# Kernel optimization log

Measured on AMD Instinct MI355X. Metric: run time of the kernel, lower is better.

The kernel has to match this reference:

```python
import jax, jax.numpy as jnp
import numpy as np

VOCAB = 32000
EMB = 512
HID = 1024
B = 64
LPRE = 256
MAXL = 16


def _gru(x, Wih, Whh, bih, bhh):
    # x: (B, T, E); torch GRU gate order r, z, n
    Bb, T, E = x.shape
    H = Whh.shape[1]
    xW = jnp.einsum('bte,ge->btg', x, Wih) + bih  # (B, T, 3H)
    def step(h, xt):
        gh = h @ Whh.T + bhh
        r = jax.nn.sigmoid(xt[:, :H] + gh[:, :H])
        z = jax.nn.sigmoid(xt[:, H:2 * H] + gh[:, H:2 * H])
        n = jnp.tanh(xt[:, 2 * H:] + r * gh[:, 2 * H:])
        h = (1.0 - z) * n + z * h
        return h, h
    h0 = jnp.zeros((Bb, H), x.dtype)
    hT, ys = jax.lax.scan(step, h0, jnp.swapaxes(xW, 0, 1))
    return jnp.swapaxes(ys, 0, 1), hT


def setup_inputs() -> dict:
    key = jax.random.key(0)
    ks = jax.random.split(key, 24)
    s = 0.02
    inp = {
        'pre_seq': jax.random.randint(ks[0], (B, LPRE), 0, VOCAB),
        'post_seq': jax.random.randint(ks[1], (B, LPRE), 0, VOCAB),
        'trg': jax.random.randint(ks[2], (B, MAXL), 0, 2),
        'emb': jax.random.normal(ks[3], (VOCAB, EMB), jnp.float32) * s,
        'Wih_pre': jax.random.normal(ks[4], (3 * HID, EMB), jnp.float32) * s,
        'Whh_pre': jax.random.normal(ks[5], (3 * HID, HID), jnp.float32) * s,
        'bih_pre': jnp.zeros((3 * HID,), jnp.float32),
        'bhh_pre': jnp.zeros((3 * HID,), jnp.float32),
        'Wih_post': jax.random.normal(ks[6], (3 * HID, EMB), jnp.float32) * s,
        'Whh_post': jax.random.normal(ks[7], (3 * HID, HID), jnp.float32) * s,
        'bih_post': jnp.zeros((3 * HID,), jnp.float32),
        'bhh_post': jnp.zeros((3 * HID,), jnp.float32),
        'fc_W': jax.random.normal(ks[8], (HID, 2 * HID), jnp.float32) * s,
        'fc_b': jnp.zeros((HID,), jnp.float32),
        'attn_W': jax.random.normal(ks[9], (HID, 2 * HID), jnp.float32) * s,
        'attn_b': jnp.zeros((HID,), jnp.float32),
        'v_W': jax.random.normal(ks[10], (1, HID), jnp.float32) * s,
        'fc1_W': jax.random.normal(ks[11], (HID, HID), jnp.float32) * s,
        'fc1_b': jnp.zeros((HID,), jnp.float32),
        'fc2_W': jax.random.normal(ks[12], (HID, 2 * HID), jnp.float32) * s,
        'fc2_b': jnp.zeros((HID,), jnp.float32),
        'fco_W': jax.random.normal(ks[13], (1, 2 * HID), jnp.float32) * s,
        'fco_b': jnp.zeros((1,), jnp.float32),
    }
    return inp


def reference(pre_seq, post_seq, trg, emb,
              Wih_pre, Whh_pre, bih_pre, bhh_pre,
              Wih_post, Whh_post, bih_post, bhh_post,
              fc_W, fc_b, attn_W, attn_b, v_W,
              fc1_W, fc1_b, fc2_W, fc2_b, fco_W, fco_b):
    bsz, len_pre = pre_seq.shape
    max_len = trg.shape[1]
    # Encoder (dropout = identity, eval mode)
    pre_e = emb[pre_seq]
    post_e = emb[post_seq]
    pre_out, pre_h = _gru(pre_e, Wih_pre, Whh_pre, bih_pre, bhh_pre)
    post_out, post_h = _gru(post_e, Wih_post, Whh_post, bih_post, bhh_post)
    enc_out = jnp.concatenate([pre_out, post_out], axis=1)  # (B, 2*Lp, H)
    hidden = jnp.tanh(jnp.concatenate([pre_h, post_h], axis=-1) @ fc_W.T + fc_b)  # (B, H)
    # Decoder: hidden is never updated in the original loop, so one step suffices;
    # the per-t result is identical and is broadcast over max_len.
    src_len = enc_out.shape[1]
    hid_rep = jnp.broadcast_to(hidden[:, None, :], (bsz, src_len, hidden.shape[-1]))
    energy = jnp.tanh(jnp.concatenate([hid_rep, enc_out], axis=-1) @ attn_W.T + attn_b)
    a = jax.nn.softmax(jnp.einsum('bsh,h->bs', energy, v_W[0]), axis=1)  # (B, S)
    weighted = jnp.einsum('bs,bsh->bh', a, enc_out)  # (B, H)
    o = jnp.tanh(hidden @ fc1_W.T + fc1_b)
    o = jnp.tanh(jnp.concatenate([o, weighted], axis=1) @ fc2_W.T + fc2_b)  # (B, H)
    o_rep = jnp.broadcast_to(o[:, None, :], (bsz, src_len, o.shape[-1]))
    feat = jax.nn.relu(jnp.concatenate([enc_out, o_rep], axis=-1))  # (B, S, 2H)
    logits = jnp.einsum('bsf,of->bso', feat, fco_W) + fco_b  # (B, S, 1)
    sig = jax.nn.sigmoid(logits)
    outputs_pre = jnp.broadcast_to(sig[:, None, :len_pre, :], (bsz, max_len, len_pre, 1))
    outputs_post = jnp.broadcast_to(sig[:, None, len_pre:, :], (bsz, max_len, len_pre, 1))
    return outputs_pre, outputs_post
```

## Files before the change

### kernel.cpp

```cpp
#include <hip/hip_runtime.h>
#include <math.h>

#define BATCH 64
#define LPRE 256
#define EMBD 512
#define HID 1024
#define G3 3072
#define SRC 512
#define CHUNK 32

typedef unsigned int uint32;
typedef unsigned long long u64;
typedef short bf16x8 __attribute__((ext_vector_type(8)));
typedef float f32x4 __attribute__((ext_vector_type(4)));
typedef uint32 u32x4 __attribute__((ext_vector_type(4)));

__device__ __forceinline__ float frcp_(float x) { return __builtin_amdgcn_rcpf(x); }
__device__ __forceinline__ float sigmoidf_(float x) {
    x = fminf(fmaxf(x, -30.f), 30.f);
    return frcp_(1.0f + __expf(-x));
}
__device__ __forceinline__ float tanhf_(float x) {
    x = fminf(fmaxf(x, -15.f), 15.f);
    float e = __expf(2.f * x);
    return (e - 1.f) * frcp_(e + 1.f);
}

__device__ __forceinline__ unsigned short f2bf(float f) {
    uint32 u = __float_as_uint(f);
    return (unsigned short)((u + 0x7fffu + ((u >> 16) & 1u)) >> 16);
}
__device__ __forceinline__ float bf2f(unsigned short s) { return __uint_as_float(((uint32)s) << 16); }
__device__ __forceinline__ uint4 pack8(float4 a, float4 b) {
    uint4 w;
    w.x = (uint32)f2bf(a.x) | ((uint32)f2bf(a.y) << 16);
    w.y = (uint32)f2bf(a.z) | ((uint32)f2bf(a.w) << 16);
    w.z = (uint32)f2bf(b.x) | ((uint32)f2bf(b.y) << 16);
    w.w = (uint32)f2bf(b.z) | ((uint32)f2bf(b.w) << 16);
    return w;
}

__global__ __launch_bounds__(256) void kcvt(const float* __restrict__ src, int ld, int off,
                                            unsigned short* __restrict__ dst, int cols, int n) {
    int i = blockIdx.x * 256 + threadIdx.x;
    if (i >= n) return;
    int r = i / cols, c = i - r * cols;
    dst[i] = f2bf(src[(size_t)r * ld + off + c]);
}

__global__ __launch_bounds__(256) void kproj(const int* __restrict__ pre_seq,
                                             const int* __restrict__ post_seq, int t0,
                                             const float* __restrict__ emb,
                                             const unsigned short* __restrict__ Wihb,
                                             const float* __restrict__ bih_pre,
                                             const float* __restrict__ bih_post,
                                             unsigned short* __restrict__ xw) {
    __shared__ uint4 Asl[4][128];
    __shared__ uint4 Bsl[4][128];
    __shared__ int tok[128];
    int gru = blockIdx.z;
    const int* seq = gru ? post_seq : pre_seq;
    const unsigned short* Wb = Wihb + (size_t)gru * G3 * EMBD;
    const float* bih = gru ? bih_post : bih_pre;
    unsigned short* xwout = xw + (size_t)gru * BATCH * CHUNK * G3;
    int tid = threadIdx.x;
    int row0 = blockIdx.x * 128, col0 = blockIdx.y * 128;
    if (tid < 128) {
        int rr = row0 + tid;
        tok[tid] = seq[(rr >> 5) * LPRE + t0 + (rr & 31)];
    }
    __syncthreads();
    int lane = tid & 63, w = tid >> 6;
    int wm = w >> 1, wn = w & 1;
    int q = lane >> 4, m = lane & 15;
    int r0s = tid & 127, g0s = tid >> 7;
    int g1s = g0s + 2;
    f32x4 acc[4][4] = {};
    for (int kk = 0; kk < EMBD; kk += 32) {
        const float* a0p = emb + (size_t)tok[r0s] * EMBD + kk + g0s * 8;
        const float* a1p = emb + (size_t)tok[r0s] * EMBD + kk + g1s * 8;
        float4 av00 = *(const float4*)a0p, av01 = *(const float4*)(a0p + 4);
        float4 av10 = *(const float4*)a1p, av11 = *(const float4*)(a1p + 4);
        uint4 bv0 = *(const uint4*)(Wb + (size_t)(col0 + r0s) * EMBD + kk + g0s * 8);
        uint4 bv1 = *(const uint4*)(Wb + (size_t)(col0 + r0s) * EMBD + kk + g1s * 8);
        __syncthreads();
        Asl[g0s][r0s ^ (g0s << 2)] = pack8(av00, av01);
        Asl[g1s][r0s ^ (g1s << 2)] = pack8(av10, av11);
        Bsl[g0s][r0s ^ (g0s << 2)] = bv0;
        Bsl[g1s][r0s ^ (g1s << 2)] = bv1;
        __syncthreads();
        bf16x8 af[4], bfv[4];
#pragma unroll
        for (int i = 0; i < 4; i++) af[i] = *(bf16x8*)&Asl[q][(wm * 64 + i * 16 + m) ^ (q << 2)];
#pragma unroll
        for (int j = 0; j < 4; j++) bfv[j] = *(bf16x8*)&Bsl[q][(wn * 64 + j * 16 + m) ^ (q << 2)];
#pragma unroll
        for (int i = 0; i < 4; i++)
#pragma unroll
            for (int j = 0; j < 4; j++)
                acc[i][j] = __builtin_amdgcn_mfma_f32_16x16x32_bf16(af[i], bfv[j], acc[i][j], 0, 0, 0);
    }
#pragma unroll
    for (int i = 0; i < 4; i++)
#pragma unroll
        for (int j = 0; j < 4; j++)
#pragma unroll
            for (int reg = 0; reg < 4; reg++) {
                int row = row0 + wm * 64 + i * 16 + q * 4 + reg;
                int col = col0 + wn * 64 + j * 16 + m;
                xwout[(size_t)row * G3 + col] = f2bf(acc[i][j][reg] + bih[col]);
            }
}

__global__ __launch_bounds__(512, 2) void kstepP(unsigned short* __restrict__ hbp,
                                                 float* __restrict__ hf,
                                                 const unsigned short* __restrict__ Whhb,
                                                 const float* __restrict__ bhh0,
                                                 const float* __restrict__ bhh1,
                                                 const unsigned short* __restrict__ xw,
                                                 unsigned short* __restrict__ enc,
                                                 uint32* __restrict__ bar,
                                                 int t0) {
    __shared__ float gl[8][32][3][17];
    __shared__ unsigned short hsh[32][16];
    int gru = blockIdx.z;
    int mh = blockIdx.y;
    int u0 = blockIdx.x * 16;
    int tid = threadIdx.x;
    int ks = tid >> 6;
    int lane = tid & 63;
    int q = lane >> 4, m = lane & 15;
    int bbase = mh * 32;
    const unsigned short* Wg = Whhb + (size_t)gru * G3 * HID;
    const float* bhh = gru ? bhh1 : bhh0;

    uint32* slots = bar + (size_t)gru * 128;
    uint32* gen = bar + 512 + (size_t)gru * 64;
    int sid = mh * 64 + blockIdx.x;
    bool leader = (sid == 0);

    bf16x8 bfrag[3][4];
#pragma unroll
    for (int g = 0; g < 3; ++g) {
        const unsigned short* pb = Wg + (size_t)(g * HID + u0 + m) * HID + ks * 128 + q * 8;
#pragma unroll
        for (int it = 0; it < 4; ++it) bfrag[g][it] = *(const bf16x8*)(pb + it * 32);
    }
#pragma unroll
    for (int g = 0; g < 3; ++g)
#pragma unroll
        for (int it = 0; it < 4; ++it) asm volatile("" : "+v"(bfrag[g][it]));

    int bl = tid >> 4, ul = tid & 15;
    int be = bbase + bl, ue = u0 + ul;
    float brr = bhh[ue], bzz = bhh[HID + ue], bnn = bhh[2 * HID + ue];
    unsigned short h16r = __hip_atomic_load(
        &hbp[(size_t)(((t0 & 1) * 2 + gru) * BATCH + be) * HID + ue],
        __ATOMIC_RELAXED, __HIP_MEMORY_SCOPE_AGENT);

    const unsigned short* xwb = xw + ((size_t)(gru * BATCH + be) * CHUNK) * G3;
    float xr = bf2f(xwb[ue]);
    float xz = bf2f(xwb[HID + ue]);
    float xn = bf2f(xwb[2 * HID + ue]);

    for (int tl = 0; tl < CHUNK; ++tl) {
        int t = t0 + tl;
        int p = t & 1;
        const unsigned short* hb = hbp + ((size_t)p * 2 + gru) * BATCH * HID;
        unsigned short* hob = hbp + ((size_t)(p ^ 1) * 2 + gru) * BATCH * HID;

        const unsigned short* pa0 = hb + (size_t)(bbase + m) * HID + ks * 128 + q * 8;
        const unsigned short* pa1 = pa0 + (size_t)16 * HID;
        u32x4 av0[4], av1[4];
#pragma unroll
        for (int it = 0; it < 4; ++it) {
            asm volatile("global_load_dwordx4 %0, %1, off sc0 sc1"
                         : "=v"(av0[it]) : "v"(pa0 + it * 32));
            asm volatile("global_load_dwordx4 %0, %1, off sc0 sc1"
                         : "=v"(av1[it]) : "v"(pa1 + it * 32));
        }
        asm volatile("s_waitcnt vmcnt(0)" ::: "memory");
        __builtin_amdgcn_sched_barrier(0);

        f32x4 acc[3][2] = {};
#pragma unroll
        for (int it = 0; it < 4; ++it)
#pragma unroll
            for (int g = 0; g < 3; ++g) {
                acc[g][0] = __builtin_amdgcn_mfma_f32_16x16x32_bf16(*(bf16x8*)&av0[it], bfrag[g][it], acc[g][0], 0, 0, 0);
                acc[g][1] = __builtin_amdgcn_mfma_f32_16x16x32_bf16(*(bf16x8*)&av1[it], bfrag[g][it], acc[g][1], 0, 0, 0);
            }
#pragma unroll
        for (int g = 0; g < 3; ++g)
#pragma unroll
            for (int reg = 0; reg < 4; ++reg) {
                gl[ks][q * 4 + reg][g][m] = acc[g][0][reg];
                gl[ks][16 + q * 4 + reg][g][m] = acc[g][1][reg];
            }
        __syncthreads();
        float ar = 0.f, az = 0.f, an = 0.f;
#pragma unroll
        for (int k2 = 0; k2 < 8; ++k2) {
            ar += gl[k2][bl][0][ul];
            az += gl[k2][bl][1][ul];
            an += gl[k2][bl][2][ul];
        }
        float r = sigmoidf_(xr + ar + brr);
        float z = sigmoidf_(xz + az + bzz);
        float n = tanhf_(xn + r * (an + bnn));
        float hnew = (1.f - z) * n + z * bf2f(h16r);
        unsigned short h16 = f2bf(hnew);
        h16r = h16;
        hsh[bl][ul] = h16;
        enc[((size_t)be * SRC + gru * LPRE + t) * HID + ue] = h16;
        if (t == LPRE - 1) hf[((size_t)gru * BATCH + be) * HID + ue] = hnew;
        __syncthreads();
        if (tid < 64) {
            int row = tid >> 1, half = tid & 1;
            u32x4 hv = *(const u32x4*)&hsh[row][half * 8];
            unsigned short* dst = hob + (size_t)(bbase + row) * HID + u0 + half * 8;
            asm volatile("global_store_dwordx4 %0, %1, off sc0 sc1"
                         :: "v"(dst), "v"(hv) : "memory");
        }
        if (tl < CHUNK - 1) {
            uint32 t1 = (uint32)(t + 1);
            if (tid < 64)
                asm volatile("s_waitcnt vmcnt(0)" ::: "memory");
            if (tid == 0)
                __hip_atomic_store(&slots[sid], t1, __ATOMIC_RELAXED, __HIP_MEMORY_SCOPE_AGENT);
            const unsigned short* xwn = xwb + (size_t)(tl + 1) * G3;
            xr = bf2f(xwn[ue]);
            xz = bf2f(xwn[HID + ue]);
            xn = bf2f(xwn[2 * HID + ue]);
            if (leader && tid < 64) {
                for (;;) {
                    uint32 s0 = __hip_atomic_load(&slots[tid], __ATOMIC_RELAXED, __HIP_MEMORY_SCOPE_AGENT);
                    uint32 s1 = __hip_atomic_load(&slots[tid + 64], __ATOMIC_RELAXED, __HIP_MEMORY_SCOPE_AGENT);
                    bool ok = (s0 >= t1) && (s1 >= t1);
                    if (__all(ok)) break;
                    __builtin_amdgcn_s_sleep(2);
                }
                if (tid == 0)
                    __hip_atomic_store(gen, t1, __ATOMIC_RELAXED, __HIP_MEMORY_SCOPE_AGENT);
            }
            if (tid == 0) {
                while (__hip_atomic_load(gen, __ATOMIC_RELAXED, __HIP_MEMORY_SCOPE_AGENT) < t1)
                    __builtin_amdgcn_s_sleep(2);
            }
            __syncthreads();
        }
    }
}

__global__ __launch_bounds__(256) void kg64(const float* __restrict__ A1, int K1,
                                            const float* __restrict__ A2, int K2,
                                            const unsigned short* __restrict__ Wb,
                                            const float* __restrict__ bias,
                                            float* __restrict__ out, int N, int act) {
    __shared__ uint4 Asl[4][64];
    int tid = threadIdx.x;
    int col0 = blockIdx.x * 64;
    int lane = tid & 63, w = tid >> 6;
    int q = lane >> 4, m = lane & 15;
    int K = K1 + K2;
    int arow = tid >> 2, akg = tid & 3;
    const unsigned short* wp = Wb + (size_t)(col0 + w * 16 + m) * K + q * 8;
    f32x4 acc[4] = {};
    for (int kk = 0; kk < K; kk += 32) {
        int k0 = kk + akg * 8;
        const float* ap = (k0 < K1) ? (A1 + (size_t)arow * K1 + k0)
                                    : (A2 + (size_t)arow * K2 + (k0 - K1));
        float4 v0 = *(const float4*)ap;
        float4 v1 = *(const float4*)(ap + 4);
        __syncthreads();
        Asl[akg][arow ^ (akg << 2)] = pack8(v0, v1);
        __syncthreads();
        bf16x8 bfv = *(const bf16x8*)(wp + kk);
        bf16x8 af[4];
#pragma unroll
        for (int i = 0; i < 4; i++) af[i] = *(bf16x8*)&Asl[q][(i * 16 + m) ^ (q << 2)];
#pragma unroll
        for (int i = 0; i < 4; i++)
            acc[i] = __builtin_amdgcn_mfma_f32_16x16x32_bf16(af[i], bfv, acc[i], 0, 0, 0);
    }
    int j = col0 + w * 16 + m;
    float bv = bias ? bias[j] : 0.f;
#pragma unroll
    for (int i = 0; i < 4; i++)
#pragma unroll
        for (int reg = 0; reg < 4; reg++) {
            int b = i * 16 + q * 4 + reg;
            float v = acc[i][reg] + bv;
            if (act == 1) v = tanhf_(v);
            out[(size_t)b * N + j] = v;
        }
}

__global__ __launch_bounds__(256) void kattn(const unsigned short* __restrict__ enc,
                                             const unsigned short* __restrict__ Wb,
                                             const float* __restrict__ attn_b,
                                             const float* __restrict__ hidA,
                                             const float* __restrict__ vW,
                                             float* __restrict__ e) {
    __shared__ uint4 Asl[4][128];
    __shared__ uint4 Bsl[4][128];
    __shared__ float red[2][128][17];
    int tid = threadIdx.x;
    int row0 = blockIdx.x * 128, col0 = blockIdx.y * 128;
    int lane = tid & 63, w = tid >> 6;
    int wm = w >> 1, wn = w & 1;
    int q = lane >> 4, m = lane & 15;
    int r0s = tid & 127, g0s = tid >> 7;
    int g1s = g0s + 2;
    f32x4 acc[4][4] = {};
    for (int kk = 0; kk < HID; kk += 32) {
        uint4 av0 = *(const uint4*)(enc + (size_t)(row0 + r0s) * HID + kk + g0s * 8);
        uint4 av1 = *(const uint4*)(enc + (size_t)(row0 + r0s) * HID + kk + g1s * 8);
        uint4 bv0 = *(const uint4*)(Wb + (size_t)(col0 + r0s) * HID + kk + g0s * 8);
        uint4 bv1 = *(const uint4*)(Wb + (size_t)(col0 + r0s) * HID + kk + g1s * 8);
        __syncthreads();
        Asl[g0s][r0s ^ (g0s << 2)] = av0;
        Asl[g1s][r0s ^ (g1s << 2)] = av1;
        Bsl[g0s][r0s ^ (g0s << 2)] = bv0;
        Bsl[g1s][r0s ^ (g1s << 2)] = bv1;
        __syncthreads();
        bf16x8 af[4], bfv[4];
#pragma unroll
        for (int i = 0; i < 4; i++) af[i] = *(bf16x8*)&Asl[q][(wm * 64 + i * 16 + m) ^ (q << 2)];
#pragma unroll
        for (int j = 0; j < 4; j++) bfv[j] = *(bf16x8*)&Bsl[q][(wn * 64 + j * 16 + m) ^ (q << 2)];
#pragma unroll
        for (int i = 0; i < 4; i++)
#pragma unroll
            for (int j = 0; j < 4; j++)
                acc[i][j] = __builtin_amdgcn_mfma_f32_16x16x32_bf16(af[i], bfv[j], acc[i][j], 0, 0, 0);
    }
    int b = row0 / SRC;
#pragma unroll
    for (int i = 0; i < 4; i++)
#pragma unroll
        for (int reg = 0; reg < 4; reg++) {
            int row_local = wm * 64 + i * 16 + q * 4 + reg;
            float s = 0.f;
#pragma unroll
            for (int j = 0; j < 4; j++) {
                int col = col0 + wn * 64 + j * 16 + m;
                float v = acc[i][j][reg] + hidA[(size_t)b * HID + col] + attn_b[col];
                s += vW[col] * tanhf(v);
            }
            red[wn][row_local][m] = s;
        }
    __syncthreads();
    if (tid < 128) {
        float s = 0.f;
        for (int c = 0; c < 16; c++) s += red[0][tid][c] + red[1][tid][c];
        atomicAdd(e + row0 + tid, s);
    }
}

__global__ __launch_bounds__(256) void ksoftmax(const float* __restrict__ e, float* __restrict__ a) {
    int b = blockIdx.x;
    int tid = threadIdx.x;
    __shared__ float red[256];
    float v0 = e[(size_t)b * SRC + tid], v1 = e[(size_t)b * SRC + 256 + tid];
    red[tid] = fmaxf(v0, v1);
    __syncthreads();
    for (int st = 128; st > 0; st >>= 1) {
        if (tid < st) red[tid] = fmaxf(red[tid], red[tid + st]);
        __syncthreads();
    }
    float mx = red[0];
    __syncthreads();
    float e0 = __expf(v0 - mx), e1 = __expf(v1 - mx);
    red[tid] = e0 + e1;
    __syncthreads();
    for (int st = 128; st > 0; st >>= 1) {
        if (tid < st) red[tid] += red[tid + st];
        __syncthreads();
    }
    float inv = 1.0f / red[0];
    a[(size_t)b * SRC + tid] = e0 * inv;
    a[(size_t)b * SRC + 256 + tid] = e1 * inv;
}

__global__ __launch_bounds__(256) void kweighted(const float* __restrict__ a,
                                                 const unsigned short* __restrict__ enc,
                                                 float* __restrict__ wout) {
    int b = blockIdx.y;
    int h = blockIdx.x * 256 + threadIdx.x;
    __shared__ float as[512];
    for (int l = threadIdx.x; l < 512; l += 256) as[l] = a[(size_t)b * SRC + l];
    __syncthreads();
    float acc = 0.f;
    for (int s = 0; s < SRC; s++) acc += as[s] * bf2f(enc[((size_t)b * SRC + s) * HID + h]);
    wout[(size_t)b * HID + h] = acc;
}

__global__ __launch_bounds__(256) void koc(const float* __restrict__ o2,
                                           const float* __restrict__ fcoW,
                                           float* __restrict__ oc) {
    int b = blockIdx.x;
    int tid = threadIdx.x;
    __shared__ float red[256];
    float s = 0.f;
    for (int j = tid; j < HID; j += 256) s += fmaxf(o2[(size_t)b * HID + j], 0.f) * fcoW[HID + j];
    red[tid] = s;
    __syncthreads();
    for (int st = 128; st > 0; st >>= 1) {
        if (tid < st) red[tid] += red[tid + st];
        __syncthreads();
    }
    if (tid == 0) oc[b] = red[0];
}

__global__ __launch_bounds__(256) void kfinal(const unsigned short* __restrict__ enc,
                                              const float* __restrict__ fcoW,
                                              const float* __restrict__ fcob,
                                              const float* __restrict__ oc,
                                              float* __restrict__ out) {
    int s = blockIdx.x;
    int b = blockIdx.y;
    int tid = threadIdx.x;
    __shared__ float red[256];
    const unsigned short* er = enc + ((size_t)b * SRC + s) * HID;
    float acc = 0.f;
    for (int h = tid; h < HID; h += 256) acc += fmaxf(bf2f(er[h]), 0.f) * fcoW[h];
    red[tid] = acc;
    __syncthreads();
    for (int st = 128; st > 0; st >>= 1) {
        if (tid < st) red[tid] += red[tid + st];
        __syncthreads();
    }
    if (tid == 0) {
        float logit = red[0] + oc[b] + fcob[0];
        float sig = 1.f / (1.f + __expf(-logit));
        size_t base = (s < LPRE) ? ((size_t)b * 16 * 256 + s)
                                 : (262144 + (size_t)b * 16 * 256 + (s - 256));
        for (int l = 0; l < 16; l++) out[base + (size_t)l * 256] = sig;
    }
}

extern "C" void kernel_launch(void* const* d_in, const int* in_sizes, int n_in,
                              void* d_out, int out_size, void* d_ws, size_t ws_size,
                              hipStream_t stream) {
    (void)in_sizes; (void)n_in; (void)out_size; (void)ws_size;
    const int* pre_seq = (const int*)d_in[0];
    const int* post_seq = (const int*)d_in[1];
    const float* emb = (const float*)d_in[3];
    const float* Wih_pre = (const float*)d_in[4];
    const float* Whh_pre = (const float*)d_in[5];
    const float* bih_pre = (const float*)d_in[6];
    const float* bhh_pre = (const float*)d_in[7];
    const float* Wih_post = (const float*)d_in[8];
    const float* Whh_post = (const float*)d_in[9];
    const float* bih_post = (const float*)d_in[10];
    const float* bhh_post = (const float*)d_in[11];
    const float* fc_W = (const float*)d_in[12];
    const float* fc_b = (const float*)d_in[13];
    const float* attn_W = (const float*)d_in[14];
    const float* attn_b = (const float*)d_in[15];
    const float* v_W = (const float*)d_in[16];
    const float* fc1_W = (const float*)d_in[17];
    const float* fc1_b = (const float*)d_in[18];
    const float* fc2_W = (const float*)d_in[19];
    const float* fc2_b = (const float*)d_in[20];
    const float* fco_W = (const float*)d_in[21];
    const float* fco_b = (const float*)d_in[22];
    float* out = (float*)d_out;

    char* ws = (char*)d_ws;
    unsigned short* xw = (unsigned short*)ws;     ws += (size_t)2 * BATCH * CHUNK * G3 * 2;
    unsigned short* enc = (unsigned short*)ws;    ws += (size_t)BATCH * SRC * HID * 2;
    unsigned short* hbp = (unsigned short*)ws;    ws += (size_t)2 * 2 * BATCH * HID * 2;
    float* hf = (float*)ws;                       ws += (size_t)2 * BATCH * HID * 4;
    unsigned short* Wihb = (unsigned short*)ws;   ws += (size_t)2 * G3 * EMBD * 2;
    unsigned short* Whhb = (unsigned short*)ws;   ws += (size_t)2 * G3 * HID * 2;
    unsigned short* attnWb = (unsigned short*)ws; ws += (size_t)HID * HID * 2;
    unsigned short* attnWa = (unsigned short*)ws; ws += (size_t)HID * HID * 2;
    unsigned short* fcWb = (unsigned short*)ws;   ws += (size_t)HID * 2 * HID * 2;
    unsigned short* fc1b = (unsigned short*)ws;   ws += (size_t)HID * HID * 2;
    unsigned short* fc2b = (unsigned short*)ws;   ws += (size_t)HID * 2 * HID * 2;
    uint32* bar = (uint32*)ws;                    ws += 4096;
    float* hidden = (float*)ws;                   ws += (size_t)BATCH * HID * 4;
    float* hidA = (float*)ws;                     ws += (size_t)BATCH * HID * 4;
    float* evec = (float*)ws;                     ws += (size_t)BATCH * SRC * 4;
    float* avec = (float*)ws;                     ws += (size_t)BATCH * SRC * 4;
    float* wsum = (float*)ws;                     ws += (size_t)BATCH * HID * 4;
    float* o1 = (float*)ws;                       ws += (size_t)BATCH * HID * 4;
    float* o2 = (float*)ws;                       ws += (size_t)BATCH * HID * 4;
    float* oc = (float*)ws;                       ws += (size_t)BATCH * 4;

    hipMemsetAsync(hbp, 0, (size_t)2 * 2 * BATCH * HID * 2, stream);
    hipMemsetAsync(evec, 0, (size_t)BATCH * SRC * 4, stream);
    hipMemsetAsync(bar, 0, 4096, stream);

    {
        int n1 = G3 * EMBD;
        kcvt<<<(n1 + 255) / 256, 256, 0, stream>>>(Wih_pre, EMBD, 0, Wihb, EMBD, n1);
        kcvt<<<(n1 + 255) / 256, 256, 0, stream>>>(Wih_post, EMBD, 0, Wihb + (size_t)G3 * EMBD, EMBD, n1);
        int n2 = G3 * HID;
        kcvt<<<(n2 + 255) / 256, 256, 0, stream>>>(Whh_pre, HID, 0, Whhb, HID, n2);
        kcvt<<<(n2 + 255) / 256, 256, 0, stream>>>(Whh_post, HID, 0, Whhb + (size_t)G3 * HID, HID, n2);
        int n3 = HID * HID;
        kcvt<<<(n3 + 255) / 256, 256, 0, stream>>>(attn_W, 2 * HID, HID, attnWb, HID, n3);
        kcvt<<<(n3 + 255) / 256, 256, 0, stream>>>(attn_W, 2 * HID, 0, attnWa, HID, n3);
        kcvt<<<(n3 + 255) / 256, 256, 0, stream>>>(fc1_W, HID, 0, fc1b, HID, n3);
        int n4 = HID * 2 * HID;
        kcvt<<<(n4 + 255) / 256, 256, 0, stream>>>(fc_W, 2 * HID, 0, fcWb, 2 * HID, n4);
        kcvt<<<(n4 + 255) / 256, 256, 0, stream>>>(fc2_W, 2 * HID, 0, fc2b, 2 * HID, n4);
    }

    for (int c = 0; c < LPRE / CHUNK; c++) {
        kproj<<<dim3(BATCH * CHUNK / 128, G3 / 128, 2), 256, 0, stream>>>(
            pre_seq, post_seq, c * CHUNK, emb, Wihb, bih_pre, bih_post, xw);
        kstepP<<<dim3(64, 2, 2), 512, 0, stream>>>(hbp, hf, Whhb, bhh_pre, bhh_post,
                                                   xw, enc, bar, c * CHUNK);
    }
    float* pre_h = hf;
    float* post_h = hf + (size_t)BATCH * HID;

    kg64<<<HID / 64, 256, 0, stream>>>(pre_h, HID, post_h, HID, fcWb, fc_b, hidden, HID, 1);
    kg64<<<HID / 64, 256, 0, stream>>>(hidden, HID, (const float*)nullptr, 0, attnWa,
                                       (const float*)nullptr, hidA, HID, 0);
    kattn<<<dim3(BATCH * SRC / 128, HID / 128), 256, 0, stream>>>(enc, attnWb, attn_b, hidA, v_W, evec);
    ksoftmax<<<BATCH, 256, 0, stream>>>(evec, avec);
    kweighted<<<dim3(HID / 256, BATCH), 256, 0, stream>>>(avec, enc, wsum);
    kg64<<<HID / 64, 256, 0, stream>>>(hidden, HID, (const float*)nullptr, 0, fc1b, fc1_b, o1, HID, 1);
    kg64<<<HID / 64, 256, 0, stream>>>(o1, HID, wsum, HID, fc2b, fc2_b, o2, HID, 1);
    koc<<<BATCH, 256, 0, stream>>>(o2, fco_W, oc);
    kfinal<<<dim3(SRC, BATCH), 256, 0, stream>>>(enc, fco_W, fco_b, oc, out);
}
```

Baseline: 2.049 ms.

## Split GRU grid barrier per batch half, enlarge chunk, fuse final relu-dot into attention

The grid barrier in the recurrent step kernel is split into four independent domains, one per GRU and batch half, each waiting on 64 blocks instead of 128. The spin sleep is also shortened. The time chunk grows to 64 when the workspace allows it, which halves the number of projection and step launches. The relu(enc)·fco_W dot product now runs inside the attention GEMM from the staged LDS tiles, replacing the separate kfinal kernel with a small elementwise output kernel. The price is extra work in one column of attention blocks and a chunk size that depends on workspace size.

```diff
diff --git a/kernel.cpp b/kernel.cpp
--- a/kernel.cpp
+++ b/kernel.cpp
@@ -7,7 +7,6 @@
 #define HID 1024
 #define G3 3072
 #define SRC 512
-#define CHUNK 32
 
 typedef unsigned int uint32;
 typedef unsigned long long u64;
@@ -31,6 +30,10 @@
     return (unsigned short)((u + 0x7fffu + ((u >> 16) & 1u)) >> 16);
 }
 __device__ __forceinline__ float bf2f(unsigned short s) { return __uint_as_float(((uint32)s) << 16); }
+__device__ __forceinline__ void up2(uint32 u, float& f0, float& f1) {
+    f0 = __uint_as_float(u << 16);
+    f1 = __uint_as_float(u & 0xffff0000u);
+}
 __device__ __forceinline__ uint4 pack8(float4 a, float4 b) {
     uint4 w;
     w.x = (uint32)f2bf(a.x) | ((uint32)f2bf(a.y) << 16);
@@ -54,7 +57,7 @@
                                              const unsigned short* __restrict__ Wihb,
                                              const float* __restrict__ bih_pre,
                                              const float* __restrict__ bih_post,
-                                             unsigned short* __restrict__ xw) {
+                                             unsigned short* __restrict__ xw, int chunk) {
     __shared__ uint4 Asl[4][128];
     __shared__ uint4 Bsl[4][128];
     __shared__ int tok[128];
@@ -62,12 +65,12 @@
     const int* seq = gru ? post_seq : pre_seq;
     const unsigned short* Wb = Wihb + (size_t)gru * G3 * EMBD;
     const float* bih = gru ? bih_post : bih_pre;
-    unsigned short* xwout = xw + (size_t)gru * BATCH * CHUNK * G3;
+    unsigned short* xwout = xw + (size_t)gru * BATCH * chunk * G3;
     int tid = threadIdx.x;
     int row0 = blockIdx.x * 128, col0 = blockIdx.y * 128;
     if (tid < 128) {
         int rr = row0 + tid;
-        tok[tid] = seq[(rr >> 5) * LPRE + t0 + (rr & 31)];
+        tok[tid] = seq[(rr / chunk) * LPRE + t0 + (rr % chunk)];
     }
     __syncthreads();
     int lane = tid & 63, w = tid >> 6;
@@ -120,7 +123,7 @@
                                                  const unsigned short* __restrict__ xw,
                                                  unsigned short* __restrict__ enc,
                                                  uint32* __restrict__ bar,
-                                                 int t0) {
+                                                 int t0, int chunk) {
     __shared__ float gl[8][32][3][17];
     __shared__ unsigned short hsh[32][16];
     int gru = blockIdx.z;
@@ -134,10 +137,11 @@
     const unsigned short* Wg = Whhb + (size_t)gru * G3 * HID;
     const float* bhh = gru ? bhh1 : bhh0;
 
-    uint32* slots = bar + (size_t)gru * 128;
-    uint32* gen = bar + 512 + (size_t)gru * 64;
-    int sid = mh * 64 + blockIdx.x;
-    bool leader = (sid == 0);
+    int dom = gru * 2 + mh;
+    uint32* slots = bar + (size_t)dom * 128;
+    uint32* gen = bar + 512 + (size_t)dom * 32;
+    int sid = blockIdx.x;
+    bool leader = (blockIdx.x == 0);
 
     bf16x8 bfrag[3][4];
 #pragma unroll
@@ -158,12 +162,12 @@
         &hbp[(size_t)(((t0 & 1) * 2 + gru) * BATCH + be) * HID + ue],
         __ATOMIC_RELAXED, __HIP_MEMORY_SCOPE_AGENT);
 
-    const unsigned short* xwb = xw + ((size_t)(gru * BATCH + be) * CHUNK) * G3;
+    const unsigned short* xwb = xw + ((size_t)(gru * BATCH + be) * chunk) * G3;
     float xr = bf2f(xwb[ue]);
     float xz = bf2f(xwb[HID + ue]);
     float xn = bf2f(xwb[2 * HID + ue]);
 
-    for (int tl = 0; tl < CHUNK; ++tl) {
+    for (int tl = 0; tl < chunk; ++tl) {
         int t = t0 + tl;
         int p = t & 1;
         const unsigned short* hb = hbp + ((size_t)p * 2 + gru) * BATCH * HID;
@@ -222,7 +226,7 @@
             asm volatile("global_store_dwordx4 %0, %1, off sc0 sc1"
                          :: "v"(dst), "v"(hv) : "memory");
         }
-        if (tl < CHUNK - 1) {
+        if (tl < chunk - 1) {
             uint32 t1 = (uint32)(t + 1);
             if (tid < 64)
                 asm volatile("s_waitcnt vmcnt(0)" ::: "memory");
@@ -235,17 +239,15 @@
             if (leader && tid < 64) {
                 for (;;) {
                     uint32 s0 = __hip_atomic_load(&slots[tid], __ATOMIC_RELAXED, __HIP_MEMORY_SCOPE_AGENT);
-                    uint32 s1 = __hip_atomic_load(&slots[tid + 64], __ATOMIC_RELAXED, __HIP_MEMORY_SCOPE_AGENT);
-                    bool ok = (s0 >= t1) && (s1 >= t1);
-                    if (__all(ok)) break;
-                    __builtin_amdgcn_s_sleep(2);
+                    if (__all(s0 >= t1)) break;
+                    __builtin_amdgcn_s_sleep(1);
                 }
                 if (tid == 0)
                     __hip_atomic_store(gen, t1, __ATOMIC_RELAXED, __HIP_MEMORY_SCOPE_AGENT);
             }
             if (tid == 0) {
                 while (__hip_atomic_load(gen, __ATOMIC_RELAXED, __HIP_MEMORY_SCOPE_AGENT) < t1)
-                    __builtin_amdgcn_s_sleep(2);
+                    __builtin_amdgcn_s_sleep(1);
             }
             __syncthreads();
         }
@@ -301,18 +303,26 @@
                                              const float* __restrict__ attn_b,
                                              const float* __restrict__ hidA,
                                              const float* __restrict__ vW,
-                                             float* __restrict__ e) {
+                                             const float* __restrict__ fcoW,
+                                             float* __restrict__ e,
+                                             float* __restrict__ dvec) {
     __shared__ uint4 Asl[4][128];
     __shared__ uint4 Bsl[4][128];
     __shared__ float red[2][128][17];
+    __shared__ float dred[128][2];
+    __shared__ float fsh[HID];
     int tid = threadIdx.x;
     int row0 = blockIdx.x * 128, col0 = blockIdx.y * 128;
+    bool dwork = (blockIdx.y == 0);
+    if (dwork)
+        for (int l = tid; l < HID; l += 256) fsh[l] = fcoW[l];
     int lane = tid & 63, w = tid >> 6;
     int wm = w >> 1, wn = w & 1;
     int q = lane >> 4, m = lane & 15;
     int r0s = tid & 127, g0s = tid >> 7;
     int g1s = g0s + 2;
     f32x4 acc[4][4] = {};
+    float dacc = 0.f;
     for (int kk = 0; kk < HID; kk += 32) {
         uint4 av0 = *(const uint4*)(enc + (size_t)(row0 + r0s) * HID + kk + g0s * 8);
         uint4 av1 = *(const uint4*)(enc + (size_t)(row0 + r0s) * HID + kk + g1s * 8);
@@ -329,6 +339,22 @@
         for (int i = 0; i < 4; i++) af[i] = *(bf16x8*)&Asl[q][(wm * 64 + i * 16 + m) ^ (q << 2)];
 #pragma unroll
         for (int j = 0; j < 4; j++) bfv[j] = *(bf16x8*)&Bsl[q][(wn * 64 + j * 16 + m) ^ (q << 2)];
+        if (dwork) {
+            int r2 = tid >> 1, sp = tid & 1;
+#pragma unroll
+            for (int sg = 0; sg < 2; sg++) {
+                int seg = sp * 2 + sg;
+                uint4 v = Asl[seg][r2 ^ (seg << 2)];
+                const uint32* vw = (const uint32*)&v;
+#pragma unroll
+                for (int wd = 0; wd < 4; wd++) {
+                    float e0, e1;
+                    up2(vw[wd], e0, e1);
+                    int kb = kk + seg * 8 + wd * 2;
+                    dacc += fmaxf(e0, 0.f) * fsh[kb] + fmaxf(e1, 0.f) * fsh[kb + 1];
+                }
+            }
+        }
 #pragma unroll
         for (int i = 0; i < 4; i++)
 #pragma unroll
@@ -350,11 +376,13 @@
             }
             red[wn][row_local][m] = s;
         }
+    if (dwork) dred[tid >> 1][tid & 1] = dacc;
     __syncthreads();
     if (tid < 128) {
         float s = 0.f;
         for (int c = 0; c < 16; c++) s += red[0][tid][c] + red[1][tid][c];
         atomicAdd(e + row0 + tid, s);
+        if (dwork) dvec[row0 + tid] = dred[tid][0] + dred[tid][1];
     }
 }
 
@@ -413,37 +441,23 @@
     if (tid == 0) oc[b] = red[0];
 }
 
-__global__ __launch_bounds__(256) void kfinal(const unsigned short* __restrict__ enc,
-                                              const float* __restrict__ fcoW,
-                                              const float* __restrict__ fcob,
-                                              const float* __restrict__ oc,
-                                              float* __restrict__ out) {
-    int s = blockIdx.x;
-    int b = blockIdx.y;
-    int tid = threadIdx.x;
-    __shared__ float red[256];
-    const unsigned short* er = enc + ((size_t)b * SRC + s) * HID;
-    float acc = 0.f;
-    for (int h = tid; h < HID; h += 256) acc += fmaxf(bf2f(er[h]), 0.f) * fcoW[h];
-    red[tid] = acc;
-    __syncthreads();
-    for (int st = 128; st > 0; st >>= 1) {
-        if (tid < st) red[tid] += red[tid + st];
-        __syncthreads();
-    }
-    if (tid == 0) {
-        float logit = red[0] + oc[b] + fcob[0];
-        float sig = 1.f / (1.f + __expf(-logit));
-        size_t base = (s < LPRE) ? ((size_t)b * 16 * 256 + s)
-                                 : (262144 + (size_t)b * 16 * 256 + (s - 256));
-        for (int l = 0; l < 16; l++) out[base + (size_t)l * 256] = sig;
-    }
+__global__ __launch_bounds__(256) void kout(const float* __restrict__ dvec,
+                                            const float* __restrict__ oc,
+                                            const float* __restrict__ fcob,
+                                            float* __restrict__ out) {
+    int idx = blockIdx.x * 256 + threadIdx.x;
+    int b = idx >> 9, s = idx & 511;
+    float logit = dvec[idx] + oc[b] + fcob[0];
+    float sig = frcp_(1.f + __expf(-fminf(fmaxf(logit, -30.f), 30.f)));
+    size_t base = (s < LPRE) ? ((size_t)b * 4096 + s)
+                             : (262144 + (size_t)b * 4096 + (s - 256));
+    for (int l = 0; l < 16; l++) out[base + (size_t)l * 256] = sig;
 }
 
 extern "C" void kernel_launch(void* const* d_in, const int* in_sizes, int n_in,
                               void* d_out, int out_size, void* d_ws, size_t ws_size,
                               hipStream_t stream) {
-    (void)in_sizes; (void)n_in; (void)out_size; (void)ws_size;
+    (void)in_sizes; (void)n_in; (void)out_size;
     const int* pre_seq = (const int*)d_in[0];
     const int* post_seq = (const int*)d_in[1];
     const float* emb = (const float*)d_in[3];
@@ -468,8 +482,11 @@
     const float* fco_b = (const float*)d_in[22];
     float* out = (float*)d_out;
 
+    const size_t fixed_bytes = 103420160ull + 65536;
+    int CH = (ws_size >= fixed_bytes + (size_t)2 * BATCH * 64 * G3 * 2) ? 64 : 32;
+
     char* ws = (char*)d_ws;
-    unsigned short* xw = (unsigned short*)ws;     ws += (size_t)2 * BATCH * CHUNK * G3 * 2;
+    unsigned short* xw = (unsigned short*)ws;     ws += (size_t)2 * BATCH * CH * G3 * 2;
     unsigned short* enc = (unsigned short*)ws;    ws += (size_t)BATCH * SRC * HID * 2;
     unsigned short* hbp = (unsigned short*)ws;    ws += (size_t)2 * 2 * BATCH * HID * 2;
     float* hf = (float*)ws;                       ws += (size_t)2 * BATCH * HID * 4;
@@ -481,6 +498,7 @@
     unsigned short* fc1b = (unsigned short*)ws;   ws += (size_t)HID * HID * 2;
     unsigned short* fc2b = (unsigned short*)ws;   ws += (size_t)HID * 2 * HID * 2;
     uint32* bar = (uint32*)ws;                    ws += 4096;
+    float* dvec = (float*)ws;                     ws += (size_t)BATCH * SRC * 4;
     float* hidden = (float*)ws;                   ws += (size_t)BATCH * HID * 4;
     float* hidA = (float*)ws;                     ws += (size_t)BATCH * HID * 4;
     float* evec = (float*)ws;                     ws += (size_t)BATCH * SRC * 4;
@@ -510,11 +528,11 @@
         kcvt<<<(n4 + 255) / 256, 256, 0, stream>>>(fc2_W, 2 * HID, 0, fc2b, 2 * HID, n4);
     }
 
-    for (int c = 0; c < LPRE / CHUNK; c++) {
-        kproj<<<dim3(BATCH * CHUNK / 128, G3 / 128, 2), 256, 0, stream>>>(
-            pre_seq, post_seq, c * CHUNK, emb, Wihb, bih_pre, bih_post, xw);
+    for (int c = 0; c < LPRE / CH; c++) {
+        kproj<<<dim3(BATCH * CH / 128, G3 / 128, 2), 256, 0, stream>>>(
+            pre_seq, post_seq, c * CH, emb, Wihb, bih_pre, bih_post, xw, CH);
         kstepP<<<dim3(64, 2, 2), 512, 0, stream>>>(hbp, hf, Whhb, bhh_pre, bhh_post,
-                                                   xw, enc, bar, c * CHUNK);
+                                                   xw, enc, bar, c * CH, CH);
     }
     float* pre_h = hf;
     float* post_h = hf + (size_t)BATCH * HID;
@@ -522,11 +540,12 @@
     kg64<<<HID / 64, 256, 0, stream>>>(pre_h, HID, post_h, HID, fcWb, fc_b, hidden, HID, 1);
     kg64<<<HID / 64, 256, 0, stream>>>(hidden, HID, (const float*)nullptr, 0, attnWa,
                                        (const float*)nullptr, hidA, HID, 0);
-    kattn<<<dim3(BATCH * SRC / 128, HID / 128), 256, 0, stream>>>(enc, attnWb, attn_b, hidA, v_W, evec);
+    kattn<<<dim3(BATCH * SRC / 128, HID / 128), 256, 0, stream>>>(enc, attnWb, attn_b, hidA,
+                                                                  v_W, fco_W, evec, dvec);
     ksoftmax<<<BATCH, 256, 0, stream>>>(evec, avec);
     kweighted<<<dim3(HID / 256, BATCH), 256, 0, stream>>>(avec, enc, wsum);
     kg64<<<HID / 64, 256, 0, stream>>>(hidden, HID, (const float*)nullptr, 0, fc1b, fc1_b, o1, HID, 1);
     kg64<<<HID / 64, 256, 0, stream>>>(o1, HID, wsum, HID, fc2b, fc2_b, o2, HID, 1);
     koc<<<BATCH, 256, 0, stream>>>(o2, fco_W, oc);
-    kfinal<<<dim3(SRC, BATCH), 256, 0, stream>>>(enc, fco_W, fco_b, oc, out);
-}
+    kout<<<BATCH * SRC / 256, 256, 0, stream>>>(dvec, oc, fco_b, out);
+}
```

Measured after the change: 1.982 ms, median of 2. 1.03x faster.
